# Optimization experiments

Measured on AMD Instinct MI355X. Metric: run time of the kernel, lower is better.

## Reference

```python
import jax, jax.numpy as jnp
import numpy as np

DIM = 128   # dim
KS = 3      # kernel_size
N = 8       # temporal frames (hard-coded n=8 in module)
B = 4       # clip batch -> 2D batch = B*N = 32
H = W = 64
EPS = 1e-5

def _bn(x, g, b, m, v):
    # inference BatchNorm2d over channel axis 1 (NCHW)
    s = g * jax.lax.rsqrt(v + EPS)
    return x * s[None, :, None, None] + (b - m * s)[None, :, None, None]

def _bn_vec(x, g, b, m, v):
    # BatchNorm over last axis of (B, C)
    s = g * jax.lax.rsqrt(v + EPS)
    return x * s + (b - m * s)

def setup_inputs():
    key = jax.random.key(0)
    ks = iter(jax.random.split(key, 48))
    nrm = lambda shape, sc=0.05: jax.random.normal(next(ks), shape, jnp.float32) * sc
    uni = lambda shape: jax.random.uniform(next(ks), shape, jnp.float32, minval=0.5, maxval=1.5)
    def bn_p(c):
        return uni((c,)), nrm((c,)), nrm((c,)), uni((c,))  # gamma, beta, running_mean, running_var
    d = {}
    d["x"] = jax.random.normal(next(ks), (B * N, DIM, H, W), jnp.float32)
    d["w_key"] = nrm((DIM, DIM // 4, KS, 1, 1))                      # conv3d (k,1,1), groups=4, no bias
    d["bnk_g"], d["bnk_b"], d["bnk_m"], d["bnk_v"] = bn_p(DIM)
    d["w_e1"] = nrm((DIM // 2, 2 * DIM))                             # 1x1 conv, no bias
    d["bne_g"], d["bne_b"], d["bne_m"], d["bne_v"] = bn_p(DIM // 2)
    d["w_e2"] = nrm((KS * DIM // 4, DIM // 2))
    d["b_e2"] = nrm((KS * DIM // 4,))
    d["gn_g"] = uni((KS * DIM // 4,))
    d["gn_b"] = nrm((KS * DIM // 4,))
    d["w_1x1"] = nrm((DIM, DIM))                                     # 1x1 conv, no bias
    d["bn1_g"], d["bn1_b"], d["bn1_m"], d["bn1_v"] = bn_p(DIM)
    d["bn2_g"], d["bn2_b"], d["bn2_m"], d["bn2_v"] = bn_p(DIM)
    d["w_se1"] = nrm((DIM, DIM))                                     # attn_chs = max(dim*2//2, 32) = dim
    d["b_se1"] = nrm((DIM,))
    d["bnse_g"], d["bnse_b"], d["bnse_m"], d["bnse_v"] = bn_p(DIM)
    d["w_se2"] = nrm((2 * DIM, DIM))
    d["b_se2"] = nrm((2 * DIM,))
    return d

def reference(x, w_key, bnk_g, bnk_b, bnk_m, bnk_v, w_e1, bne_g, bne_b, bne_m, bne_v,
              w_e2, b_e2, gn_g, gn_b, w_1x1, bn1_g, bn1_b, bn1_m, bn1_v,
              bn2_g, bn2_b, bn2_m, bn2_v, w_se1, b_se1, bnse_g, bnse_b, bnse_m, bnse_v,
              w_se2, b_se2):
    B2, C, Hh, Ww = x.shape
    b = B2 // N
    # --- key_embed: temporal grouped conv3d + BN + ReLU ---
    x5 = x.reshape(b, N, C, Hh, Ww).transpose(0, 2, 1, 3, 4)          # b c n h w
    kk = jax.lax.conv_general_dilated(
        x5, w_key, (1, 1, 1), ((KS // 2, KS // 2), (0, 0), (0, 0)),
        dimension_numbers=('NCDHW', 'OIDHW', 'NCDHW'), feature_group_count=4)
    k2d = kk.transpose(0, 2, 1, 3, 4).reshape(B2, C, Hh, Ww)
    k2d = jax.nn.relu(_bn(k2d, bnk_g, bnk_b, bnk_m, bnk_v))
    # --- dynamic per-pixel temporal kernels ---
    qk = jnp.concatenate([x, k2d], axis=1)                            # (b n) 2c h w
    e = jax.nn.relu(_bn(jnp.einsum('bchw,oc->bohw', qk, w_e1), bne_g, bne_b, bne_m, bne_v))
    wd = jnp.einsum('bchw,oc->bohw', e, w_e2) + b_e2[None, :, None, None]
    # GroupNorm: num_groups = C//4, group size = KS channels -> normalize over (KS, H, W)
    wg = wd.reshape(B2, C // 4, KS, Hh, Ww)
    mu = wg.mean(axis=(2, 3, 4), keepdims=True)
    var = wg.var(axis=(2, 3, 4), keepdims=True)
    wg = (wg - mu) * jax.lax.rsqrt(var + EPS)
    wd = wg.reshape(B2, KS * C // 4, Hh, Ww) * gn_g[None, :, None, None] + gn_b[None, :, None, None]
    wd = wd.reshape(B2, C // 4, KS, Hh, Ww)                           # w.view(b, c//4, 1, k, h, w) with c-dim squeezed
    # --- value path: 1x1 conv + BN, temporal unfold, dynamic aggregation ---
    v = _bn(jnp.einsum('bchw,oc->bohw', x, w_1x1), bn1_g, bn1_b, bn1_m, bn1_v)
    v5 = v.reshape(b, N, C, Hh, Ww).transpose(0, 2, 1, 3, 4)          # b c n h w
    pf = (KS - 1) // 2
    vp = jnp.pad(v5, ((0, 0), (0, 0), (pf, KS - 1 - pf), (0, 0), (0, 0)))
    unf = jnp.stack([vp[:, :, i:i + N] for i in range(KS)], axis=-1)  # b c n h w k (unfold dim=2)
    unf = unf.transpose(0, 2, 1, 3, 4, 5).reshape(B2, C // 4, 4, Hh, Ww, KS)  # (b n) c1 c2 h w k
    agg = jnp.einsum('nckhw,ncdhwk->ncdhw', wd, unf).reshape(B2, C, Hh, Ww)
    agg = _bn(agg, bn2_g, bn2_b, bn2_m, bn2_v)
    agg = agg * jax.nn.sigmoid(agg)                                   # SiLU
    # --- radix-2 split attention over (agg, k) ---
    x6 = agg.reshape(b, N, C, Hh, Ww).transpose(0, 2, 1, 3, 4)        # B C N H W
    k6 = k2d.reshape(b, N, C, Hh, Ww).transpose(0, 2, 1, 3, 4)
    u = jnp.stack([x6, k6], axis=2)                                   # B C 2 N H W
    gap = u.sum(axis=2).mean(axis=(2, 3, 4))                          # B C
    a = jax.nn.relu(_bn_vec(gap @ w_se1.T + b_se1, bnse_g, bnse_b, bnse_m, bnse_v))
    attn = jax.nn.softmax((a @ w_se2.T + b_se2).reshape(b, C, 2), axis=2)
    out = (u * attn[:, :, :, None, None, None]).sum(axis=2)           # B C N H W
    return out.transpose(0, 2, 1, 3, 4).reshape(B2, C, Hh, Ww)
```

## Files before the change

### kernel.cpp

```cpp
#include <hip/hip_runtime.h>

#define EPSV 1e-5f
typedef unsigned short u16;
typedef unsigned int u32;


typedef __attribute__((ext_vector_type(8))) __bf16 bf16x8;
typedef __attribute__((ext_vector_type(4))) float f32x4;
union ABcast { uint4 u; bf16x8 v; };

__device__ __forceinline__ u32 bfbits(float f) {
    u32 u = __float_as_uint(f);
    u += 0x7fff + ((u >> 16) & 1);
    return u >> 16;
}
__device__ __forceinline__ float bflo(u32 p) { return __uint_as_float(p << 16); }
__device__ __forceinline__ float bfhi(u32 p) { return __uint_as_float(p & 0xffff0000u); }

__global__ __launch_bounds__(256) void kW_pack(
    const float* __restrict__ wk, const float* __restrict__ w1,
    const float* __restrict__ we1, const float* __restrict__ we2,
    u32* __restrict__ wkF, u32* __restrict__ wB1,
    u32* __restrict__ wB, u32* __restrict__ wB2,
    float* __restrict__ stats_zero)
{
    int i = blockIdx.x * 256 + threadIdx.x;
    if (i < 2560) stats_zero[i] = 0.f;
    if (i < 6144) {
        int jj = i & 3;
        int ln = (i >> 2) & 63;
        int nt = (i >> 8) & 1;
        int rest = i >> 9;
        int grp = rest / 3, dk = rest % 3;
        int n = nt * 16 + (ln & 15);
        int k = (ln >> 4) * 8 + 2 * jj;
        int o = grp * 32 + n;
        wkF[i] = bfbits(wk[o * 96 + k * 3 + dk]) |
                 (bfbits(wk[o * 96 + (k + 1) * 3 + dk]) << 16);
    } else if (i < 14336) {
        int j2 = i - 6144;
        int jj = j2 & 3;
        int ln = (j2 >> 2) & 63;
        int nt = (j2 >> 8) & 7;
        int kb = j2 >> 11;
        int n = nt * 16 + (ln & 15);
        int k = kb * 32 + (ln >> 4) * 8 + 2 * jj;
        wB1[j2] = bfbits(w1[n * 128 + k]) | (bfbits(w1[n * 128 + k + 1]) << 16);
    } else if (i < 22528) {
        int j2 = i - 14336;
        int jj = j2 & 3;
        int ln = (j2 >> 2) & 63;
        int nt = (j2 >> 8) & 3;
        int kb = j2 >> 10;
        int n  = nt * 16 + (ln & 15);
        int k  = kb * 32 + (ln >> 4) * 8 + 2 * jj;
        wB[j2] = bfbits(we1[n * 256 + k]) | (bfbits(we1[n * 256 + k + 1]) << 16);
    } else if (i < 25600) {
        int j2 = i - 22528;
        int jj = j2 & 3;
        int ln = (j2 >> 2) & 63;
        int rest = j2 >> 8;
        int kb = rest / 6, nt = rest % 6;
        int n = nt * 16 + (ln & 15);
        int k = kb * 32 + (ln >> 4) * 8 + 2 * jj;
        wB2[j2] = bfbits(we2[n * 64 + k]) | (bfbits(we2[n * 64 + k + 1]) << 16);
    }
}

__global__ __launch_bounds__(256, 8) void kX_cvt(
    const float* __restrict__ x, u32* __restrict__ xq)
{
    int qid = blockIdx.x * 256 + threadIdx.x;
    int px  = qid & 4095;
    int c8g = qid >> 12;
    const float* xp = x + (c8g * 8) * 4096 + px;
    uint4 o;
    o.x = bfbits(xp[0])        | (bfbits(xp[4096])     << 16);
    o.y = bfbits(xp[2 * 4096]) | (bfbits(xp[3 * 4096]) << 16);
    o.z = bfbits(xp[4 * 4096]) | (bfbits(xp[5 * 4096]) << 16);
    o.w = bfbits(xp[6 * 4096]) | (bfbits(xp[7 * 4096]) << 16);
    *(uint4*)(xq + (c8g * 4096 + px) * 4) = o;
}

__global__ __launch_bounds__(256, 4) void kA_key(
    const u32* __restrict__ xq, const u32* __restrict__ wkF,
    const float* __restrict__ g, const float* __restrict__ bb,
    const float* __restrict__ m, const float* __restrict__ vr,
    u32* __restrict__ k2dh2, float* __restrict__ gap)
{
    int tid  = threadIdx.x;
    int lane = tid & 63;
    int q    = __builtin_amdgcn_readfirstlane(tid >> 6);
    int blk  = blockIdx.x;
    int tile = blk & 15;
    int grp  = (blk >> 4) & 3;
    int b2   = blk >> 6;
    int px0  = tile * 256;
    int bi = b2 >> 3, ni = b2 & 7;
    int lrow = lane & 15, lk = lane >> 4;
    const uint4* wkF4 = (const uint4*)wkF;

    f32x4 acc[4][2];
    #pragma unroll
    for (int mt = 0; mt < 4; ++mt)
        #pragma unroll
        for (int nt = 0; nt < 2; ++nt)
            acc[mt][nt] = (f32x4){0.f, 0.f, 0.f, 0.f};

    int pxA[4];
    #pragma unroll
    for (int mt = 0; mt < 4; ++mt) pxA[mt] = px0 + (4 * q + mt) * 16 + lrow;

    #pragma unroll
    for (int dk = 0; dk < 3; ++dk) {
        int nf = ni + dk - 1;
        if (nf >= 0 && nf < 8) {
            const u32* src = xq + (((bi * 8 + nf) * 16 + grp * 4 + lk) * 4096) * 4;
            ABcast a[4];
            #pragma unroll
            for (int mt = 0; mt < 4; ++mt)
                a[mt].u = *(const uint4*)(src + pxA[mt] * 4);
            #pragma unroll
            for (int nt = 0; nt < 2; ++nt) {
                ABcast bfr;
                bfr.u = wkF4[((grp * 3 + dk) * 2 + nt) * 64 + lane];
                #pragma unroll
                for (int mt = 0; mt < 4; ++mt)
                    acc[mt][nt] = __builtin_amdgcn_mfma_f32_16x16x32_bf16(
                        a[mt].v, bfr.v, acc[mt][nt], 0, 0, 0);
            }
        }
    }

    __shared__ float ssum[32][4];
    #pragma unroll
    for (int nt = 0; nt < 2; ++nt) {
        int ch = grp * 32 + nt * 16 + lrow;
        float s = g[ch] * rsqrtf(vr[ch] + EPSV);
        float t = bb[ch] - m[ch] * s;
        float lsum = 0.f;
        #pragma unroll
        for (int mt = 0; mt < 4; ++mt) {
            float r0 = fmaxf(fmaf(acc[mt][nt].x, s, t), 0.f);
            float r1 = fmaxf(fmaf(acc[mt][nt].y, s, t), 0.f);
            float r2 = fmaxf(fmaf(acc[mt][nt].z, s, t), 0.f);
            float r3 = fmaxf(fmaf(acc[mt][nt].w, s, t), 0.f);
            lsum += r0 + r1 + r2 + r3;
            float p0 = __shfl_xor(r0, 1, 64);
            float p1 = __shfl_xor(r1, 1, 64);
            float p2 = __shfl_xor(r2, 1, 64);
            float p3 = __shfl_xor(r3, 1, 64);
            if (!(lane & 1)) {
                int c2out = grp * 16 + nt * 8 + (lrow >> 1);
                uint4 pk;
                pk.x = bfbits(r0) | (bfbits(p0) << 16);
                pk.y = bfbits(r1) | (bfbits(p1) << 16);
                pk.z = bfbits(r2) | (bfbits(p2) << 16);
                pk.w = bfbits(r3) | (bfbits(p3) << 16);
                *(uint4*)(k2dh2 + (b2 * 64 + c2out) * 4096 +
                          px0 + (4 * q + mt) * 16 + lk * 4) = pk;
            }
        }
        lsum += __shfl_xor(lsum, 16, 64);
        lsum += __shfl_xor(lsum, 32, 64);
        if (lane < 16) ssum[nt * 16 + lrow][q] = lsum;
    }
    __syncthreads();
    if (tid < 32) {
        float* sr = ssum[tid];
        atomicAdd(&gap[bi * 128 + grp * 32 + tid], sr[0] + sr[1] + sr[2] + sr[3]);
    }
}

__global__ __launch_bounds__(256, 3) void kB_val(
    const u32* __restrict__ xq, const u32* __restrict__ wB1,
    const float* __restrict__ g, const float* __restrict__ bb,
    const float* __restrict__ m, const float* __restrict__ vr,
    u16* __restrict__ vh)
{
    int tid  = threadIdx.x;
    int lane = tid & 63;
    int q    = __builtin_amdgcn_readfirstlane(tid >> 6);
    int tile = blockIdx.x & 31;
    int b2   = blockIdx.x >> 5;
    int px0  = tile * 128;
    int lrow = lane & 15, lk = lane >> 4;

    const uint4* wB14 = (const uint4*)wB1;

    f32x4 acc[2][8];
    #pragma unroll
    for (int mt = 0; mt < 2; ++mt)
        #pragma unroll
        for (int nt = 0; nt < 8; ++nt)
            acc[mt][nt] = (f32x4){0.f, 0.f, 0.f, 0.f};

    int pxA0 = px0 + (2 * q) * 16 + lrow;
    int pxA1 = pxA0 + 16;

    #pragma unroll
    for (int kblk = 0; kblk < 4; ++kblk) {
        const u32* src = xq + ((b2 * 16 + kblk * 4 + lk) * 4096) * 4;
        ABcast a0, a1;
        a0.u = *(const uint4*)(src + pxA0 * 4);
        a1.u = *(const uint4*)(src + pxA1 * 4);
        #pragma unroll
        for (int nt = 0; nt < 8; ++nt) {
            ABcast bfr;
            bfr.u = wB14[(kblk * 8 + nt) * 64 + lane];
            acc[0][nt] = __builtin_amdgcn_mfma_f32_16x16x32_bf16(a0.v, bfr.v, acc[0][nt], 0, 0, 0);
            acc[1][nt] = __builtin_amdgcn_mfma_f32_16x16x32_bf16(a1.v, bfr.v, acc[1][nt], 0, 0, 0);
        }
    }

    #pragma unroll
    for (int nt = 0; nt < 8; ++nt) {
        int ch = nt * 16 + lrow;
        float s = g[ch] * rsqrtf(vr[ch] + EPSV);
        float t = bb[ch] - m[ch] * s;
        #pragma unroll
        for (int mt = 0; mt < 2; ++mt) {
            float r0 = fmaf(acc[mt][nt].x, s, t);
            float r1 = fmaf(acc[mt][nt].y, s, t);
            float r2 = fmaf(acc[mt][nt].z, s, t);
            float r3 = fmaf(acc[mt][nt].w, s, t);
            uint2 pk;
            pk.x = bfbits(r0) | (bfbits(r1) << 16);
            pk.y = bfbits(r2) | (bfbits(r3) << 16);
            *(uint2*)(vh + (b2 * 128 + ch) * 4096 +
                      px0 + (2 * q + mt) * 16 + lk * 4) = pk;
        }
    }
}

__global__ __launch_bounds__(256, 3) void kC_wd(
    const u32* __restrict__ xq, const u32* __restrict__ k2dh2,
    const u32* __restrict__ wB,
    const float* __restrict__ eg, const float* __restrict__ eb,
    const float* __restrict__ em, const float* __restrict__ ev,
    const u32* __restrict__ wB2, const float* __restrict__ be2,
    u16* __restrict__ wdh, float* __restrict__ gnsum, float* __restrict__ gnsq)
{
    int tid  = threadIdx.x;
    int lane = tid & 63;
    int q    = __builtin_amdgcn_readfirstlane(tid >> 6);
    int tile = blockIdx.x & 31;
    int b2   = blockIdx.x >> 5;
    int px0  = tile * 128;
    int lrow = lane & 15;
    int lk   = lane >> 4;

    const u32* kb = k2dh2 + b2 * 64 * 4096;
    const uint4* wB4 = (const uint4*)wB;

    f32x4 acc[2][4];
    #pragma unroll
    for (int mt = 0; mt < 2; ++mt)
        #pragma unroll
        for (int nt = 0; nt < 4; ++nt)
            acc[mt][nt] = (f32x4){0.f, 0.f, 0.f, 0.f};

    int pxA0 = px0 + (2 * q) * 16 + lrow;
    int pxA1 = pxA0 + 16;

    #pragma unroll
    for (int kblk = 0; kblk < 4; ++kblk) {
        const u32* src = xq + ((b2 * 16 + kblk * 4 + lk) * 4096) * 4;
        ABcast a0, a1;
        a0.u = *(const uint4*)(src + pxA0 * 4);
        a1.u = *(const uint4*)(src + pxA1 * 4);
        #pragma unroll
        for (int nt = 0; nt < 4; ++nt) {
            ABcast bfr;
            bfr.u = wB4[(kblk * 4 + nt) * 64 + lane];
            acc[0][nt] = __builtin_amdgcn_mfma_f32_16x16x32_bf16(a0.v, bfr.v, acc[0][nt], 0, 0, 0);
            acc[1][nt] = __builtin_amdgcn_mfma_f32_16x16x32_bf16(a1.v, bfr.v, acc[1][nt], 0, 0, 0);
        }
    }
    #pragma unroll
    for (int kblk = 4; kblk < 8; ++kblk) {
        int c2b = (((kblk & 3) * 16) + lk * 4) * 4096;
        ABcast a0, a1;
        a0.u.x = kb[c2b         + pxA0];
        a0.u.y = kb[c2b + 4096  + pxA0];
        a0.u.z = kb[c2b + 8192  + pxA0];
        a0.u.w = kb[c2b + 12288 + pxA0];
        a1.u.x = kb[c2b         + pxA1];
        a1.u.y = kb[c2b + 4096  + pxA1];
        a1.u.z = kb[c2b + 8192  + pxA1];
        a1.u.w = kb[c2b + 12288 + pxA1];
        #pragma unroll
        for (int nt = 0; nt < 4; ++nt) {
            ABcast bfr;
            bfr.u = wB4[(kblk * 4 + nt) * 64 + lane];
            acc[0][nt] = __builtin_amdgcn_mfma_f32_16x16x32_bf16(a0.v, bfr.v, acc[0][nt], 0, 0, 0);
            acc[1][nt] = __builtin_amdgcn_mfma_f32_16x16x32_bf16(a1.v, bfr.v, acc[1][nt], 0, 0, 0);
        }
    }

    __shared__ __align__(16) u32 e_s2[32][132];
    #pragma unroll
    for (int nt = 0; nt < 4; ++nt) {
        int ch = nt * 16 + lrow;
        float s = eg[ch] * rsqrtf(ev[ch] + EPSV);
        float t = eb[ch] - em[ch] * s;
        #pragma unroll
        for (int mt = 0; mt < 2; ++mt) {
            float r0 = fmaxf(fmaf(acc[mt][nt].x, s, t), 0.f);
            float r1 = fmaxf(fmaf(acc[mt][nt].y, s, t), 0.f);
            float r2 = fmaxf(fmaf(acc[mt][nt].z, s, t), 0.f);
            float r3 = fmaxf(fmaf(acc[mt][nt].w, s, t), 0.f);
            float p0 = __shfl_xor(r0, 1, 64);
            float p1 = __shfl_xor(r1, 1, 64);
            float p2 = __shfl_xor(r2, 1, 64);
            float p3 = __shfl_xor(r3, 1, 64);
            if (!(lane & 1)) {
                uint4 pk;
                pk.x = bfbits(r0) | (bfbits(p0) << 16);
                pk.y = bfbits(r1) | (bfbits(p1) << 16);
                pk.z = bfbits(r2) | (bfbits(p2) << 16);
                pk.w = bfbits(r3) | (bfbits(p3) << 16);
                *(uint4*)&e_s2[nt * 8 + (lrow >> 1)][(2 * q + mt) * 16 + lk * 4] = pk;
            }
        }
    }
    __syncthreads();

    const uint4* wB24 = (const uint4*)wB2;
    f32x4 acc2[2][6];
    #pragma unroll
    for (int mt = 0; mt < 2; ++mt)
        #pragma unroll
        for (int nt = 0; nt < 6; ++nt)
            acc2[mt][nt] = (f32x4){0.f, 0.f, 0.f, 0.f};

    #pragma unroll
    for (int kb2 = 0; kb2 < 2; ++kb2) {
        int c2r = kb2 * 16 + lk * 4;
        ABcast a0, a1;
        int pl0 = (2 * q) * 16 + lrow;
        int pl1 = pl0 + 16;
        a0.u.x = e_s2[c2r + 0][pl0];
        a0.u.y = e_s2[c2r + 1][pl0];
        a0.u.z = e_s2[c2r + 2][pl0];
        a0.u.w = e_s2[c2r + 3][pl0];
        a1.u.x = e_s2[c2r + 0][pl1];
        a1.u.y = e_s2[c2r + 1][pl1];
        a1.u.z = e_s2[c2r + 2][pl1];
        a1.u.w = e_s2[c2r + 3][pl1];
        #pragma unroll
        for (int nt = 0; nt < 6; ++nt) {
            ABcast bfr;
            bfr.u = wB24[(kb2 * 6 + nt) * 64 + lane];
            acc2[0][nt] = __builtin_amdgcn_mfma_f32_16x16x32_bf16(a0.v, bfr.v, acc2[0][nt], 0, 0, 0);
            acc2[1][nt] = __builtin_amdgcn_mfma_f32_16x16x32_bf16(a1.v, bfr.v, acc2[1][nt], 0, 0, 0);
        }
    }

    __shared__ float s_sum[96][4], s_sq[96][4];
    #pragma unroll
    for (int nt = 0; nt < 6; ++nt) {
        int ch = nt * 16 + lrow;
        float bias = be2[ch];
        float lsum = 0.f, lsq = 0.f;
        #pragma unroll
        for (int mt = 0; mt < 2; ++mt) {
            float v0 = acc2[mt][nt].x + bias;
            float v1 = acc2[mt][nt].y + bias;
            float v2 = acc2[mt][nt].z + bias;
            float v3 = acc2[mt][nt].w + bias;
            uint2 pk;
            pk.x = bfbits(v0) | (bfbits(v1) << 16);
            pk.y = bfbits(v2) | (bfbits(v3) << 16);
            *(uint2*)(wdh + (b2 * 96 + ch) * 4096 +
                      px0 + (2 * q + mt) * 16 + lk * 4) = pk;
            lsum += v0 + v1 + v2 + v3;
            lsq  += v0 * v0 + v1 * v1 + v2 * v2 + v3 * v3;
        }
        lsum += __shfl_xor(lsum, 16, 64);
        lsum += __shfl_xor(lsum, 32, 64);
        lsq  += __shfl_xor(lsq, 16, 64);
        lsq  += __shfl_xor(lsq, 32, 64);
        if (lane < 16) { s_sum[ch][q] = lsum; s_sq[ch][q] = lsq; }
    }
    __syncthreads();
    if (tid < 32) {
        float ss = 0.f, sq = 0.f;
        #pragma unroll
        for (int j = 0; j < 3; ++j) {
            int ch = tid * 3 + j;
            ss += s_sum[ch][0] + s_sum[ch][1] + s_sum[ch][2] + s_sum[ch][3];
            sq += s_sq[ch][0] + s_sq[ch][1] + s_sq[ch][2] + s_sq[ch][3];
        }
        atomicAdd(&gnsum[b2 * 32 + tid], ss);
        atomicAdd(&gnsq [b2 * 32 + tid], sq);
    }
}

__global__ __launch_bounds__(256) void kC2_gn(
    const float* __restrict__ gnsum, const float* __restrict__ gnsq,
    float* __restrict__ gnmean, float* __restrict__ gnrstd)
{
    int idx = blockIdx.x * 256 + threadIdx.x;
    const float inv = 1.f / 12288.f;
    float mu  = gnsum[idx] * inv;
    float var = fmaf(gnsq[idx], inv, -mu * mu);
    gnmean[idx] = mu;
    gnrstd[idx] = rsqrtf(fmaxf(var, 0.f) + EPSV);
}

__global__ __launch_bounds__(256, 8) void kD_agg(
    const u16* __restrict__ wdh, const u16* __restrict__ vh,
    const float* __restrict__ gnmean, const float* __restrict__ gnrstd,
    const float* __restrict__ gng, const float* __restrict__ gnb,
    const float* __restrict__ g, const float* __restrict__ bb,
    const float* __restrict__ m, const float* __restrict__ vr,
    u16* __restrict__ aggh, float* __restrict__ gap)
{
    int blk   = blockIdx.x;
    int strip = blk & 7;
    int c1    = (blk >> 3) & 31;
    int bi    = blk >> 8;
    int px0   = strip * 512 + threadIdx.x * 2;

    float sch[4], tch[4], gl[4];
    #pragma unroll
    for (int ch = 0; ch < 4; ++ch) {
        int c = c1 * 4 + ch;
        float s = g[c] * rsqrtf(vr[c] + EPSV);
        sch[ch] = s; tch[ch] = bb[c] - m[c] * s; gl[ch] = 0.f;
    }
    float gg[3], gb[3];
    #pragma unroll
    for (int k = 0; k < 3; ++k) { gg[k] = gng[c1 * 3 + k]; gb[k] = gnb[c1 * 3 + k]; }

    float2 vreg[4][3];
    #pragma unroll
    for (int ch = 0; ch < 4; ++ch) {
        vreg[ch][0] = make_float2(0.f, 0.f);
        u32 v1u = *(const u32*)(vh + ((bi * 8 + 0) * 128 + c1 * 4 + ch) * 4096 + px0);
        u32 v2u = *(const u32*)(vh + ((bi * 8 + 1) * 128 + c1 * 4 + ch) * 4096 + px0);
        vreg[ch][1] = make_float2(bflo(v1u), bfhi(v1u));
        vreg[ch][2] = make_float2(bflo(v2u), bfhi(v2u));
    }

    for (int ni = 0; ni < 8; ++ni) {
        int b2 = bi * 8 + ni;
        float mu = gnmean[b2 * 32 + c1], rs = gnrstd[b2 * 32 + c1];
        float2 wn[3];
        #pragma unroll
        for (int k = 0; k < 3; ++k) {
            int nf = ni + k - 1;
            if (nf >= 0 && nf < 8) {
                u32 wvu = *(const u32*)(wdh + ((b2 * 96 + c1 * 3 + k) * 4096 + px0));
                wn[k].x = fmaf((bflo(wvu) - mu) * rs, gg[k], gb[k]);
                wn[k].y = fmaf((bfhi(wvu) - mu) * rs, gg[k], gb[k]);
            } else {
                wn[k] = make_float2(0.f, 0.f);
            }
        }
        #pragma unroll
        for (int ch = 0; ch < 4; ++ch) {
            float a0 = 0.f, a1 = 0.f;
            #pragma unroll
            for (int k = 0; k < 3; ++k) {
                a0 = fmaf(wn[k].x, vreg[ch][k].x, a0);
                a1 = fmaf(wn[k].y, vreg[ch][k].y, a1);
            }
            float y0 = fmaf(a0, sch[ch], tch[ch]);
            float y1 = fmaf(a1, sch[ch], tch[ch]);
            float r0 = y0 / (1.f + __expf(-y0));
            float r1 = y1 / (1.f + __expf(-y1));
            *(u32*)(aggh + (b2 * 128 + c1 * 4 + ch) * 4096 + px0) =
                bfbits(r0) | (bfbits(r1) << 16);
            gl[ch] += r0 + r1;
        }
        if (ni < 7) {
            #pragma unroll
            for (int ch = 0; ch < 4; ++ch) {
                vreg[ch][0] = vreg[ch][1];
                vreg[ch][1] = vreg[ch][2];
                if (ni + 2 < 8) {
                    u32 vu = *(const u32*)(vh + ((bi * 8 + ni + 2) * 128 + c1 * 4 + ch) * 4096 + px0);
                    vreg[ch][2] = make_float2(bflo(vu), bfhi(vu));
                }
            }
        }
    }

    __shared__ float sm[4][4];
    int lane = threadIdx.x & 63, wid = threadIdx.x >> 6;
    #pragma unroll
    for (int ch = 0; ch < 4; ++ch) {
        float s = gl[ch];
        #pragma unroll
        for (int off = 32; off; off >>= 1) s += __shfl_down(s, off, 64);
        if (lane == 0) sm[ch][wid] = s;
    }
    __syncthreads();
    if (threadIdx.x < 4) {
        float* sr = sm[threadIdx.x];
        atomicAdd(&gap[bi * 128 + c1 * 4 + threadIdx.x], sr[0] + sr[1] + sr[2] + sr[3]);
    }
}

__global__ __launch_bounds__(256) void kE1_a(
    const float* __restrict__ gap,
    const float* __restrict__ w1, const float* __restrict__ b1,
    const float* __restrict__ g, const float* __restrict__ bb,
    const float* __restrict__ m, const float* __restrict__ vr,
    float* __restrict__ a_buf)
{
    int idx = blockIdx.x * 256 + threadIdx.x;
    int bi = idx >> 7, oc = idx & 127;
    float acc = b1[oc];
    const float* gp = gap + bi * 128;
    const float* wp = w1 + oc * 128;
    for (int c = 0; c < 128; c += 4) {
        const float4 w4 = *(const float4*)(wp + c);
        acc = fmaf(gp[c + 0] * (1.f / 32768.f), w4.x, acc);
        acc = fmaf(gp[c + 1] * (1.f / 32768.f), w4.y, acc);
        acc = fmaf(gp[c + 2] * (1.f / 32768.f), w4.z, acc);
        acc = fmaf(gp[c + 3] * (1.f / 32768.f), w4.w, acc);
    }
    float s = g[oc] * rsqrtf(vr[oc] + EPSV);
    a_buf[bi * 128 + oc] = fmaxf(fmaf(acc, s, bb[oc] - m[oc] * s), 0.f);
}

__global__ __launch_bounds__(256) void kE2_attn(
    const float* __restrict__ a_buf,
    const float* __restrict__ w2, const float* __restrict__ b2v,
    float* __restrict__ attn)
{
    int idx = blockIdx.x * 256 + threadIdx.x;
    int bi = idx >> 7, cc = idx & 127;
    float l0 = b2v[cc * 2], l1 = b2v[cc * 2 + 1];
    const float* ap  = a_buf + bi * 128;
    const float* w0p = w2 + (cc * 2) * 128;
    const float* w1p = w2 + (cc * 2 + 1) * 128;
    for (int j = 0; j < 128; j += 4) {
        const float4 wa4 = *(const float4*)(w0p + j);
        const float4 wb4 = *(const float4*)(w1p + j);
        l0 = fmaf(ap[j + 0], wa4.x, l0); l1 = fmaf(ap[j + 0], wb4.x, l1);
        l0 = fmaf(ap[j + 1], wa4.y, l0); l1 = fmaf(ap[j + 1], wb4.y, l1);
        l0 = fmaf(ap[j + 2], wa4.z, l0); l1 = fmaf(ap[j + 2], wb4.z, l1);
        l0 = fmaf(ap[j + 3], wa4.w, l0); l1 = fmaf(ap[j + 3], wb4.w, l1);
    }
    float mx = fmaxf(l0, l1);
    float e0 = __expf(l0 - mx), e1 = __expf(l1 - mx);
    float inv = 1.f / (e0 + e1);
    attn[bi * 256 + cc * 2]     = e0 * inv;
    attn[bi * 256 + cc * 2 + 1] = e1 * inv;
}

__global__ __launch_bounds__(256, 8) void kF_out(
    float* __restrict__ out, const u16* __restrict__ aggh,
    const u32* __restrict__ k2dh2, const float* __restrict__ attn)
{
    int blk   = blockIdx.x;
    int strip = blk & 3;
    int c2    = (blk >> 2) & 63;
    int b2    = blk >> 8;
    int bi    = b2 >> 3;
    int px0   = strip * 1024 + threadIdx.x * 4;

    float a0e = attn[bi * 256 + 4 * c2];
    float a1e = attn[bi * 256 + 4 * c2 + 1];
    float a0o = attn[bi * 256 + 4 * c2 + 2];
    float a1o = attn[bi * 256 + 4 * c2 + 3];

    uint4 kk = *(const uint4*)(k2dh2 + (b2 * 64 + c2) * 4096 + px0);
    uint2 g0 = *(const uint2*)(aggh + (b2 * 128 + 2 * c2) * 4096 + px0);
    uint2 g1 = *(const uint2*)(aggh + (b2 * 128 + 2 * c2 + 1) * 4096 + px0);

    float4 re, ro;
    re.x = fmaf(a0e, bflo(g0.x), a1e * bflo(kk.x));
    re.y = fmaf(a0e, bfhi(g0.x), a1e * bflo(kk.y));
    re.z = fmaf(a0e, bflo(g0.y), a1e * bflo(kk.z));
    re.w = fmaf(a0e, bfhi(g0.y), a1e * bflo(kk.w));
    ro.x = fmaf(a0o, bflo(g1.x), a1o * bfhi(kk.x));
    ro.y = fmaf(a0o, bfhi(g1.x), a1o * bfhi(kk.y));
    ro.z = fmaf(a0o, bflo(g1.y), a1o * bfhi(kk.z));
    ro.w = fmaf(a0o, bfhi(g1.y), a1o * bfhi(kk.w));
    *(float4*)(out + (b2 * 128 + 2 * c2) * 4096 + px0) = re;
    *(float4*)(out + (b2 * 128 + 2 * c2 + 1) * 4096 + px0) = ro;
}

extern "C" void kernel_launch(void* const* d_in, const int* in_sizes, int n_in,
                              void* d_out, int out_size, void* d_ws, size_t ws_size,
                              hipStream_t stream)
{
    const float* x      = (const float*)d_in[0];
    const float* w_key  = (const float*)d_in[1];
    const float* bnk_g  = (const float*)d_in[2];
    const float* bnk_b  = (const float*)d_in[3];
    const float* bnk_m  = (const float*)d_in[4];
    const float* bnk_v  = (const float*)d_in[5];
    const float* w_e1   = (const float*)d_in[6];
    const float* bne_g  = (const float*)d_in[7];
    const float* bne_b  = (const float*)d_in[8];
    const float* bne_m  = (const float*)d_in[9];
    const float* bne_v  = (const float*)d_in[10];
    const float* w_e2   = (const float*)d_in[11];
    const float* b_e2   = (const float*)d_in[12];
    const float* gn_g   = (const float*)d_in[13];
    const float* gn_b   = (const float*)d_in[14];
    const float* w_1x1  = (const float*)d_in[15];
    const float* bn1_g  = (const float*)d_in[16];
    const float* bn1_b  = (const float*)d_in[17];
    const float* bn1_m  = (const float*)d_in[18];
    const float* bn1_v  = (const float*)d_in[19];
    const float* bn2_g  = (const float*)d_in[20];
    const float* bn2_b  = (const float*)d_in[21];
    const float* bn2_m  = (const float*)d_in[22];
    const float* bn2_v  = (const float*)d_in[23];
    const float* w_se1  = (const float*)d_in[24];
    const float* b_se1  = (const float*)d_in[25];
    const float* bnse_g = (const float*)d_in[26];
    const float* bnse_b = (const float*)d_in[27];
    const float* bnse_m = (const float*)d_in[28];
    const float* bnse_v = (const float*)d_in[29];
    const float* w_se2  = (const float*)d_in[30];
    const float* b_se2  = (const float*)d_in[31];

    float* ws    = (float*)d_ws;
    u32*  xq    = (u32*)ws;
    u32*  k2dh2 = (u32*)(ws + 8388608);
    u16*  vh    = (u16*)(ws + 16777216);
    u16*  aggh  = (u16*)(ws + 25165824);
    u16*  wdh   = (u16*)(ws + 33554432);
    u32*  wkF   = (u32*)(ws + 39845888);
    u32*  wB1   = wkF + 6144;
    u32*  wB    = wB1 + 8192;
    u32*  wB2   = wB + 8192;
    float* st   = ws + 46137344;
    float* gnsum  = st;
    float* gnsq   = st + 1024;
    float* gap    = st + 2048;
    float* gnmean = st + 2560;
    float* gnrstd = st + 3584;
    float* attn   = st + 4608;
    float* a_buf  = st;

    kW_pack<<<100, 256, 0, stream>>>(w_key, w_1x1, w_e1, w_e2, wkF, wB1, wB, wB2, gnsum);
    kX_cvt<<<8192, 256, 0, stream>>>(x, xq);
    kA_key<<<2048, 256, 0, stream>>>(xq, wkF, bnk_g, bnk_b, bnk_m, bnk_v, k2dh2, gap);
    kB_val<<<1024, 256, 0, stream>>>(xq, wB1, bn1_g, bn1_b, bn1_m, bn1_v, vh);
    kC_wd<<<1024, 256, 0, stream>>>(xq, k2dh2, wB, bne_g, bne_b, bne_m, bne_v,
                                    wB2, b_e2, wdh, gnsum, gnsq);
    kC2_gn<<<4, 256, 0, stream>>>(gnsum, gnsq, gnmean, gnrstd);
    kD_agg<<<1024, 256, 0, stream>>>(wdh, vh, gnmean, gnrstd, gn_g, gn_b,
                                     bn2_g, bn2_b, bn2_m, bn2_v, aggh, gap);
    kE1_a<<<2, 256, 0, stream>>>(gap, w_se1, b_se1, bnse_g, bnse_b, bnse_m, bnse_v, a_buf);
    kE2_attn<<<2, 256, 0, stream>>>(a_buf, w_se2, b_se2, attn);
    kF_out<<<8192, 256, 0, stream>>>((float*)d_out, aggh, k2dh2, attn);
}
```

Baseline: 150.9 us.

## Store key activations in channel-interleaved layout and merge small launch kernels

Result: faster. 136.6 us (median of 2 runs) (-9.5%).

```diff
diff --git a/kernel.cpp b/kernel.cpp
--- a/kernel.cpp
+++ b/kernel.cpp
@@ -3,7 +3,6 @@
 #define EPSV 1e-5f
 typedef unsigned short u16;
 typedef unsigned int u32;
-
 
 typedef __attribute__((ext_vector_type(8))) __bf16 bf16x8;
 typedef __attribute__((ext_vector_type(4))) float f32x4;
@@ -17,14 +16,26 @@
 __device__ __forceinline__ float bflo(u32 p) { return __uint_as_float(p << 16); }
 __device__ __forceinline__ float bfhi(u32 p) { return __uint_as_float(p & 0xffff0000u); }
 
-__global__ __launch_bounds__(256) void kW_pack(
+__global__ __launch_bounds__(256, 8) void kXW_cvt(
+    const float* __restrict__ x, u32* __restrict__ xq,
     const float* __restrict__ wk, const float* __restrict__ w1,
     const float* __restrict__ we1, const float* __restrict__ we2,
     u32* __restrict__ wkF, u32* __restrict__ wB1,
     u32* __restrict__ wB, u32* __restrict__ wB2,
     float* __restrict__ stats_zero)
 {
-    int i = blockIdx.x * 256 + threadIdx.x;
+    int qid = blockIdx.x * 256 + threadIdx.x;
+    int px  = qid & 4095;
+    int c8g = qid >> 12;
+    const float* xp = x + (c8g * 8) * 4096 + px;
+    uint4 o;
+    o.x = bfbits(xp[0])        | (bfbits(xp[4096])     << 16);
+    o.y = bfbits(xp[2 * 4096]) | (bfbits(xp[3 * 4096]) << 16);
+    o.z = bfbits(xp[4 * 4096]) | (bfbits(xp[5 * 4096]) << 16);
+    o.w = bfbits(xp[6 * 4096]) | (bfbits(xp[7 * 4096]) << 16);
+    *(uint4*)(xq + (c8g * 4096 + px) * 4) = o;
+
+    int i = qid;
     if (i < 2560) stats_zero[i] = 0.f;
     if (i < 6144) {
         int jj = i & 3;
@@ -34,9 +45,9 @@
         int grp = rest / 3, dk = rest % 3;
         int n = nt * 16 + (ln & 15);
         int k = (ln >> 4) * 8 + 2 * jj;
-        int o = grp * 32 + n;
-        wkF[i] = bfbits(wk[o * 96 + k * 3 + dk]) |
-                 (bfbits(wk[o * 96 + (k + 1) * 3 + dk]) << 16);
+        int oo = grp * 32 + n;
+        wkF[i] = bfbits(wk[oo * 96 + k * 3 + dk]) |
+                 (bfbits(wk[oo * 96 + (k + 1) * 3 + dk]) << 16);
     } else if (i < 14336) {
         int j2 = i - 6144;
         int jj = j2 & 3;
@@ -67,26 +78,11 @@
     }
 }
 
-__global__ __launch_bounds__(256, 8) void kX_cvt(
-    const float* __restrict__ x, u32* __restrict__ xq)
-{
-    int qid = blockIdx.x * 256 + threadIdx.x;
-    int px  = qid & 4095;
-    int c8g = qid >> 12;
-    const float* xp = x + (c8g * 8) * 4096 + px;
-    uint4 o;
-    o.x = bfbits(xp[0])        | (bfbits(xp[4096])     << 16);
-    o.y = bfbits(xp[2 * 4096]) | (bfbits(xp[3 * 4096]) << 16);
-    o.z = bfbits(xp[4 * 4096]) | (bfbits(xp[5 * 4096]) << 16);
-    o.w = bfbits(xp[6 * 4096]) | (bfbits(xp[7 * 4096]) << 16);
-    *(uint4*)(xq + (c8g * 4096 + px) * 4) = o;
-}
-
 __global__ __launch_bounds__(256, 4) void kA_key(
     const u32* __restrict__ xq, const u32* __restrict__ wkF,
     const float* __restrict__ g, const float* __restrict__ bb,
     const float* __restrict__ m, const float* __restrict__ vr,
-    u32* __restrict__ k2dh2, float* __restrict__ gap)
+    u32* __restrict__ k2dq, float* __restrict__ gap)
 {
     int tid  = threadIdx.x;
     int lane = tid & 63;
@@ -132,6 +128,7 @@
         }
     }
 
+    __shared__ u16  karr[32][260];
     __shared__ float ssum[32][4];
     #pragma unroll
     for (int nt = 0; nt < 2; ++nt) {
@@ -146,20 +143,12 @@
             float r2 = fmaxf(fmaf(acc[mt][nt].z, s, t), 0.f);
             float r3 = fmaxf(fmaf(acc[mt][nt].w, s, t), 0.f);
             lsum += r0 + r1 + r2 + r3;
-            float p0 = __shfl_xor(r0, 1, 64);
-            float p1 = __shfl_xor(r1, 1, 64);
-            float p2 = __shfl_xor(r2, 1, 64);
-            float p3 = __shfl_xor(r3, 1, 64);
-            if (!(lane & 1)) {
-                int c2out = grp * 16 + nt * 8 + (lrow >> 1);
-                uint4 pk;
-                pk.x = bfbits(r0) | (bfbits(p0) << 16);
-                pk.y = bfbits(r1) | (bfbits(p1) << 16);
-                pk.z = bfbits(r2) | (bfbits(p2) << 16);
-                pk.w = bfbits(r3) | (bfbits(p3) << 16);
-                *(uint4*)(k2dh2 + (b2 * 64 + c2out) * 4096 +
-                          px0 + (4 * q + mt) * 16 + lk * 4) = pk;
-            }
+            int pxl = (4 * q + mt) * 16 + lk * 4;
+            u16* kr = &karr[nt * 16 + lrow][pxl];
+            kr[0] = (u16)bfbits(r0);
+            kr[1] = (u16)bfbits(r1);
+            kr[2] = (u16)bfbits(r2);
+            kr[3] = (u16)bfbits(r3);
         }
         lsum += __shfl_xor(lsum, 16, 64);
         lsum += __shfl_xor(lsum, 32, 64);
@@ -169,6 +158,15 @@
     if (tid < 32) {
         float* sr = ssum[tid];
         atomicAdd(&gap[bi * 128 + grp * 32 + tid], sr[0] + sr[1] + sr[2] + sr[3]);
+    }
+    #pragma unroll
+    for (int c8g = 0; c8g < 4; ++c8g) {
+        uint4 pk;
+        pk.x = (u32)karr[c8g * 8 + 0][tid] | ((u32)karr[c8g * 8 + 1][tid] << 16);
+        pk.y = (u32)karr[c8g * 8 + 2][tid] | ((u32)karr[c8g * 8 + 3][tid] << 16);
+        pk.z = (u32)karr[c8g * 8 + 4][tid] | ((u32)karr[c8g * 8 + 5][tid] << 16);
+        pk.w = (u32)karr[c8g * 8 + 6][tid] | ((u32)karr[c8g * 8 + 7][tid] << 16);
+        *(uint4*)(k2dq + ((b2 * 16 + grp * 4 + c8g) * 4096 + px0 + tid) * 4) = pk;
     }
 }
 
@@ -234,7 +232,7 @@
 }
 
 __global__ __launch_bounds__(256, 3) void kC_wd(
-    const u32* __restrict__ xq, const u32* __restrict__ k2dh2,
+    const u32* __restrict__ xq, const u32* __restrict__ k2dq,
     const u32* __restrict__ wB,
     const float* __restrict__ eg, const float* __restrict__ eb,
     const float* __restrict__ em, const float* __restrict__ ev,
@@ -250,7 +248,6 @@
     int lrow = lane & 15;
     int lk   = lane >> 4;
 
-    const u32* kb = k2dh2 + b2 * 64 * 4096;
     const uint4* wB4 = (const uint4*)wB;
 
     f32x4 acc[2][4];
@@ -264,31 +261,12 @@
     int pxA1 = pxA0 + 16;
 
     #pragma unroll
-    for (int kblk = 0; kblk < 4; ++kblk) {
-        const u32* src = xq + ((b2 * 16 + kblk * 4 + lk) * 4096) * 4;
+    for (int kblk = 0; kblk < 8; ++kblk) {
+        const u32* base = (kblk < 4) ? xq : k2dq;
+        const u32* src = base + ((b2 * 16 + (kblk & 3) * 4 + lk) * 4096) * 4;
         ABcast a0, a1;
         a0.u = *(const uint4*)(src + pxA0 * 4);
         a1.u = *(const uint4*)(src + pxA1 * 4);
-        #pragma unroll
-        for (int nt = 0; nt < 4; ++nt) {
-            ABcast bfr;
-            bfr.u = wB4[(kblk * 4 + nt) * 64 + lane];
-            acc[0][nt] = __builtin_amdgcn_mfma_f32_16x16x32_bf16(a0.v, bfr.v, acc[0][nt], 0, 0, 0);
-            acc[1][nt] = __builtin_amdgcn_mfma_f32_16x16x32_bf16(a1.v, bfr.v, acc[1][nt], 0, 0, 0);
-        }
-    }
-    #pragma unroll
-    for (int kblk = 4; kblk < 8; ++kblk) {
-        int c2b = (((kblk & 3) * 16) + lk * 4) * 4096;
-        ABcast a0, a1;
-        a0.u.x = kb[c2b         + pxA0];
-        a0.u.y = kb[c2b + 4096  + pxA0];
-        a0.u.z = kb[c2b + 8192  + pxA0];
-        a0.u.w = kb[c2b + 12288 + pxA0];
-        a1.u.x = kb[c2b         + pxA1];
-        a1.u.y = kb[c2b + 4096  + pxA1];
-        a1.u.z = kb[c2b + 8192  + pxA1];
-        a1.u.w = kb[c2b + 12288 + pxA1];
         #pragma unroll
         for (int nt = 0; nt < 4; ++nt) {
             ABcast bfr;
@@ -397,21 +375,9 @@
     }
 }
 
-__global__ __launch_bounds__(256) void kC2_gn(
-    const float* __restrict__ gnsum, const float* __restrict__ gnsq,
-    float* __restrict__ gnmean, float* __restrict__ gnrstd)
-{
-    int idx = blockIdx.x * 256 + threadIdx.x;
-    const float inv = 1.f / 12288.f;
-    float mu  = gnsum[idx] * inv;
-    float var = fmaf(gnsq[idx], inv, -mu * mu);
-    gnmean[idx] = mu;
-    gnrstd[idx] = rsqrtf(fmaxf(var, 0.f) + EPSV);
-}
-
 __global__ __launch_bounds__(256, 8) void kD_agg(
     const u16* __restrict__ wdh, const u16* __restrict__ vh,
-    const float* __restrict__ gnmean, const float* __restrict__ gnrstd,
+    const float* __restrict__ gnsum, const float* __restrict__ gnsq,
     const float* __restrict__ gng, const float* __restrict__ gnb,
     const float* __restrict__ g, const float* __restrict__ bb,
     const float* __restrict__ m, const float* __restrict__ vr,
@@ -422,6 +388,7 @@
     int c1    = (blk >> 3) & 31;
     int bi    = blk >> 8;
     int px0   = strip * 512 + threadIdx.x * 2;
+    const float inv = 1.f / 12288.f;
 
     float sch[4], tch[4], gl[4];
     #pragma unroll
@@ -446,7 +413,9 @@
 
     for (int ni = 0; ni < 8; ++ni) {
         int b2 = bi * 8 + ni;
-        float mu = gnmean[b2 * 32 + c1], rs = gnrstd[b2 * 32 + c1];
+        float mu = gnsum[b2 * 32 + c1] * inv;
+        float var = fmaf(gnsq[b2 * 32 + c1], inv, -mu * mu);
+        float rs = rsqrtf(fmaxf(var, 0.f) + EPSV);
         float2 wn[3];
         #pragma unroll
         for (int k = 0; k < 3; ++k) {
@@ -504,15 +473,17 @@
     }
 }
 
-__global__ __launch_bounds__(256) void kE1_a(
+__global__ __launch_bounds__(128) void kE_attn(
     const float* __restrict__ gap,
     const float* __restrict__ w1, const float* __restrict__ b1,
     const float* __restrict__ g, const float* __restrict__ bb,
     const float* __restrict__ m, const float* __restrict__ vr,
-    float* __restrict__ a_buf)
-{
-    int idx = blockIdx.x * 256 + threadIdx.x;
-    int bi = idx >> 7, oc = idx & 127;
+    const float* __restrict__ w2, const float* __restrict__ b2v,
+    float* __restrict__ attn)
+{
+    __shared__ float a_s[128];
+    int bi = blockIdx.x;
+    int oc = threadIdx.x;
     float acc = b1[oc];
     const float* gp = gap + bi * 128;
     const float* wp = w1 + oc * 128;
@@ -524,27 +495,20 @@
         acc = fmaf(gp[c + 3] * (1.f / 32768.f), w4.w, acc);
     }
     float s = g[oc] * rsqrtf(vr[oc] + EPSV);
-    a_buf[bi * 128 + oc] = fmaxf(fmaf(acc, s, bb[oc] - m[oc] * s), 0.f);
-}
-
-__global__ __launch_bounds__(256) void kE2_attn(
-    const float* __restrict__ a_buf,
-    const float* __restrict__ w2, const float* __restrict__ b2v,
-    float* __restrict__ attn)
-{
-    int idx = blockIdx.x * 256 + threadIdx.x;
-    int bi = idx >> 7, cc = idx & 127;
+    a_s[oc] = fmaxf(fmaf(acc, s, bb[oc] - m[oc] * s), 0.f);
+    __syncthreads();
+
+    int cc = threadIdx.x;
     float l0 = b2v[cc * 2], l1 = b2v[cc * 2 + 1];
-    const float* ap  = a_buf + bi * 128;
     const float* w0p = w2 + (cc * 2) * 128;
     const float* w1p = w2 + (cc * 2 + 1) * 128;
     for (int j = 0; j < 128; j += 4) {
         const float4 wa4 = *(const float4*)(w0p + j);
         const float4 wb4 = *(const float4*)(w1p + j);
-        l0 = fmaf(ap[j + 0], wa4.x, l0); l1 = fmaf(ap[j + 0], wb4.x, l1);
-        l0 = fmaf(ap[j + 1], wa4.y, l0); l1 = fmaf(ap[j + 1], wb4.y, l1);
-        l0 = fmaf(ap[j + 2], wa4.z, l0); l1 = fmaf(ap[j + 2], wb4.z, l1);
-        l0 = fmaf(ap[j + 3], wa4.w, l0); l1 = fmaf(ap[j + 3], wb4.w, l1);
+        l0 = fmaf(a_s[j + 0], wa4.x, l0); l1 = fmaf(a_s[j + 0], wb4.x, l1);
+        l0 = fmaf(a_s[j + 1], wa4.y, l0); l1 = fmaf(a_s[j + 1], wb4.y, l1);
+        l0 = fmaf(a_s[j + 2], wa4.z, l0); l1 = fmaf(a_s[j + 2], wb4.z, l1);
+        l0 = fmaf(a_s[j + 3], wa4.w, l0); l1 = fmaf(a_s[j + 3], wb4.w, l1);
     }
     float mx = fmaxf(l0, l1);
     float e0 = __expf(l0 - mx), e1 = __expf(l1 - mx);
@@ -555,35 +519,42 @@
 
 __global__ __launch_bounds__(256, 8) void kF_out(
     float* __restrict__ out, const u16* __restrict__ aggh,
-    const u32* __restrict__ k2dh2, const float* __restrict__ attn)
+    const u32* __restrict__ k2dq, const float* __restrict__ attn)
 {
     int blk   = blockIdx.x;
     int strip = blk & 3;
-    int c2    = (blk >> 2) & 63;
-    int b2    = blk >> 8;
+    int c8    = (blk >> 2) & 15;
+    int b2    = blk >> 6;
     int bi    = b2 >> 3;
-    int px0   = strip * 1024 + threadIdx.x * 4;
-
-    float a0e = attn[bi * 256 + 4 * c2];
-    float a1e = attn[bi * 256 + 4 * c2 + 1];
-    float a0o = attn[bi * 256 + 4 * c2 + 2];
-    float a1o = attn[bi * 256 + 4 * c2 + 3];
-
-    uint4 kk = *(const uint4*)(k2dh2 + (b2 * 64 + c2) * 4096 + px0);
-    uint2 g0 = *(const uint2*)(aggh + (b2 * 128 + 2 * c2) * 4096 + px0);
-    uint2 g1 = *(const uint2*)(aggh + (b2 * 128 + 2 * c2 + 1) * 4096 + px0);
-
-    float4 re, ro;
-    re.x = fmaf(a0e, bflo(g0.x), a1e * bflo(kk.x));
-    re.y = fmaf(a0e, bfhi(g0.x), a1e * bflo(kk.y));
-    re.z = fmaf(a0e, bflo(g0.y), a1e * bflo(kk.z));
-    re.w = fmaf(a0e, bfhi(g0.y), a1e * bflo(kk.w));
-    ro.x = fmaf(a0o, bflo(g1.x), a1o * bfhi(kk.x));
-    ro.y = fmaf(a0o, bfhi(g1.x), a1o * bfhi(kk.y));
-    ro.z = fmaf(a0o, bflo(g1.y), a1o * bfhi(kk.z));
-    ro.w = fmaf(a0o, bfhi(g1.y), a1o * bfhi(kk.w));
-    *(float4*)(out + (b2 * 128 + 2 * c2) * 4096 + px0) = re;
-    *(float4*)(out + (b2 * 128 + 2 * c2 + 1) * 4096 + px0) = ro;
+    int p     = strip * 1024 + threadIdx.x * 4;
+
+    const u32* kp = k2dq + ((b2 * 16 + c8) * 4096 + p) * 4;
+    uint4 kq[4];
+    #pragma unroll
+    for (int i = 0; i < 4; ++i) kq[i] = *(const uint4*)(kp + i * 4);
+
+    #pragma unroll
+    for (int j = 0; j < 8; ++j) {
+        int ch = c8 * 8 + j;
+        float a0 = attn[bi * 256 + ch * 2];
+        float a1 = attn[bi * 256 + ch * 2 + 1];
+        uint2 ag = *(const uint2*)(aggh + (b2 * 128 + ch) * 4096 + p);
+        float av[4] = { bflo(ag.x), bfhi(ag.x), bflo(ag.y), bfhi(ag.y) };
+        float4 r;
+        u32 kd0 = (&kq[0].x)[j >> 1];
+        u32 kd1 = (&kq[1].x)[j >> 1];
+        u32 kd2 = (&kq[2].x)[j >> 1];
+        u32 kd3 = (&kq[3].x)[j >> 1];
+        float kv0 = (j & 1) ? bfhi(kd0) : bflo(kd0);
+        float kv1 = (j & 1) ? bfhi(kd1) : bflo(kd1);
+        float kv2 = (j & 1) ? bfhi(kd2) : bflo(kd2);
+        float kv3 = (j & 1) ? bfhi(kd3) : bflo(kd3);
+        r.x = fmaf(a0, av[0], a1 * kv0);
+        r.y = fmaf(a0, av[1], a1 * kv1);
+        r.z = fmaf(a0, av[2], a1 * kv2);
+        r.w = fmaf(a0, av[3], a1 * kv3);
+        *(float4*)(out + (b2 * 128 + ch) * 4096 + p) = r;
+    }
 }
 
 extern "C" void kernel_launch(void* const* d_in, const int* in_sizes, int n_in,
@@ -625,7 +596,7 @@
 
     float* ws    = (float*)d_ws;
     u32*  xq    = (u32*)ws;
-    u32*  k2dh2 = (u32*)(ws + 8388608);
+    u32*  k2dq  = (u32*)(ws + 8388608);
     u16*  vh    = (u16*)(ws + 16777216);
     u16*  aggh  = (u16*)(ws + 25165824);
     u16*  wdh   = (u16*)(ws + 33554432);
@@ -637,21 +608,17 @@
     float* gnsum  = st;
     float* gnsq   = st + 1024;
     float* gap    = st + 2048;
-    float* gnmean = st + 2560;
-    float* gnrstd = st + 3584;
     float* attn   = st + 4608;
-    float* a_buf  = st;
-
-    kW_pack<<<100, 256, 0, stream>>>(w_key, w_1x1, w_e1, w_e2, wkF, wB1, wB, wB2, gnsum);
-    kX_cvt<<<8192, 256, 0, stream>>>(x, xq);
-    kA_key<<<2048, 256, 0, stream>>>(xq, wkF, bnk_g, bnk_b, bnk_m, bnk_v, k2dh2, gap);
+
+    kXW_cvt<<<8192, 256, 0, stream>>>(x, xq, w_key, w_1x1, w_e1, w_e2,
+                                      wkF, wB1, wB, wB2, gnsum);
+    kA_key<<<2048, 256, 0, stream>>>(xq, wkF, bnk_g, bnk_b, bnk_m, bnk_v, k2dq, gap);
     kB_val<<<1024, 256, 0, stream>>>(xq, wB1, bn1_g, bn1_b, bn1_m, bn1_v, vh);
-    kC_wd<<<1024, 256, 0, stream>>>(xq, k2dh2, wB, bne_g, bne_b, bne_m, bne_v,
+    kC_wd<<<1024, 256, 0, stream>>>(xq, k2dq, wB, bne_g, bne_b, bne_m, bne_v,
                                     wB2, b_e2, wdh, gnsum, gnsq);
-    kC2_gn<<<4, 256, 0, stream>>>(gnsum, gnsq, gnmean, gnrstd);
-    kD_agg<<<1024, 256, 0, stream>>>(wdh, vh, gnmean, gnrstd, gn_g, gn_b,
+    kD_agg<<<1024, 256, 0, stream>>>(wdh, vh, gnsum, gnsq, gn_g, gn_b,
                                      bn2_g, bn2_b, bn2_m, bn2_v, aggh, gap);
-    kE1_a<<<2, 256, 0, stream>>>(gap, w_se1, b_se1, bnse_g, bnse_b, bnse_m, bnse_v, a_buf);
-    kE2_attn<<<2, 256, 0, stream>>>(a_buf, w_se2, b_se2, attn);
-    kF_out<<<8192, 256, 0, stream>>>((float*)d_out, aggh, k2dh2, attn);
-}
+    kE_attn<<<4, 128, 0, stream>>>(gap, w_se1, b_se1, bnse_g, bnse_b, bnse_m, bnse_v,
+                                   w_se2, b_se2, attn);
+    kF_out<<<2048, 256, 0, stream>>>((float*)d_out, aggh, k2dq, attn);
+}
```
